# Performance work log

Hardware: AMD Instinct MI355X
Metric: run time of the kernel (lower is better)

The kernel has to match this reference:

```python
import jax, jax.numpy as jnp
import numpy as np

B, S, D, H, FF = 2, 4096, 512, 8, 2048
HD = D // H
EPS = 1e-5


def setup_inputs() -> dict:
    key = jax.random.key(0)
    ks = jax.random.split(key, 14)
    init = lambda k, shape: jax.random.normal(k, shape, dtype=jnp.float32) * 0.02
    return {
        "x": jax.random.normal(ks[0], (B, S, D), dtype=jnp.float32),
        "Wq": init(ks[1], (D, D)), "bq": jnp.zeros((D,), jnp.float32),
        "Wk": init(ks[2], (D, D)), "bk": jnp.zeros((D,), jnp.float32),
        "Wv": init(ks[3], (D, D)), "bv": jnp.zeros((D,), jnp.float32),
        "Wo": init(ks[4], (D, D)), "bo": jnp.zeros((D,), jnp.float32),
        "W1": init(ks[5], (D, FF)), "b1": jnp.zeros((FF,), jnp.float32),
        "W2": init(ks[6], (FF, D)), "b2": jnp.zeros((D,), jnp.float32),
        "g1": jnp.ones((D,), jnp.float32), "beta1": jnp.zeros((D,), jnp.float32),
        "g2": jnp.ones((D,), jnp.float32), "beta2": jnp.zeros((D,), jnp.float32),
    }


def layer_norm(x, g, b):
    mu = jnp.mean(x, axis=-1, keepdims=True)
    var = jnp.mean(jnp.square(x - mu), axis=-1, keepdims=True)
    return (x - mu) * jax.lax.rsqrt(var + EPS) * g + b


def reference(x, Wq, bq, Wk, bk, Wv, bv, Wo, bo, W1, b1, W2, b2, g1, beta1, g2, beta2):
    # --- pre-LN self-attention block ---
    residual = x
    h = layer_norm(x, g1, beta1)
    # project and split heads: [B, H, S, HD]
    q = (h @ Wq + bq).reshape(B, S, H, HD).transpose(0, 2, 1, 3)
    k = (h @ Wk + bk).reshape(B, S, H, HD).transpose(0, 2, 1, 3)
    v = (h @ Wv + bv).reshape(B, S, H, HD).transpose(0, 2, 1, 3)
    scale = HD ** -0.5
    scores = jnp.einsum('bhqd,bhkd->bhqk', q, k) * scale  # [B,H,S,S] materialized
    attn = jax.nn.softmax(scores, axis=-1)
    ctx = jnp.einsum('bhqk,bhkd->bhqd', attn, v)
    ctx = ctx.transpose(0, 2, 1, 3).reshape(B, S, D)
    attn_out = ctx @ Wo + bo
    x = residual + attn_out  # dropout p=0.0 -> identity
    # --- pre-LN FFN block ---
    residual = x
    h = layer_norm(x, g2, beta2)
    h = jax.nn.gelu(h @ W1 + b1, approximate=False)  # nn.GELU default = exact erf
    h = h @ W2 + b2
    x = residual + h
    return (x, attn)
```

## Files before the change

### kernel.cpp

```cpp
#include <hip/hip_runtime.h>
#include <hip/hip_bf16.h>

#define B_ 2
#define S_ 4096
#define D_ 512
#define H_ 8
#define HD_ 64
#define FF_ 2048
#define NT_ (B_*S_)
#define EPS_ 1e-5f

typedef __attribute__((ext_vector_type(8))) short bf16x8;
typedef __attribute__((ext_vector_type(4))) float f32x4;
typedef __attribute__((ext_vector_type(4))) unsigned int u32x4;

__device__ __forceinline__ short f2bf(float f){
  __hip_bfloat16 h = __float2bfloat16(f);
  return __builtin_bit_cast(short, h);
}
__device__ __forceinline__ float bf2f(short s){
  return __bfloat162float(__builtin_bit_cast(__hip_bfloat16, s));
}
__device__ __forceinline__ unsigned pack2(float lo, float hi){
  return ((unsigned)(unsigned short)f2bf(hi) << 16) | (unsigned short)f2bf(lo);
}
__device__ __forceinline__ void load8(const float* p, float* f){
  f32x4 a = *(const f32x4*)p; f32x4 b = *(const f32x4*)(p+4);
  #pragma unroll
  for (int j=0;j<4;j++){ f[j]=a[j]; f[4+j]=b[j]; }
}
__device__ __forceinline__ void load8(const short* p, float* f){
  bf16x8 v = *(const bf16x8*)p;
  #pragma unroll
  for (int j=0;j<8;j++) f[j]=bf2f(v[j]);
}
__device__ __forceinline__ float ldval(const float* p, size_t i){ return p[i]; }
__device__ __forceinline__ float ldval(const short* p, size_t i){ return bf2f(p[i]); }
__device__ __forceinline__ void stval(float* p, size_t i, float v){ p[i]=v; }
__device__ __forceinline__ void stval(short* p, size_t i, float v){ p[i]=f2bf(v); }

#define GLL(src, dst) __builtin_amdgcn_global_load_lds( \
    (const __attribute__((address_space(1))) void*)(src), \
    (__attribute__((address_space(3))) void*)(dst), 16, 0, 0)

__global__ __launch_bounds__(256) void transpose_bf(const float* __restrict__ W,
                                                    short* __restrict__ WT, int K, int N){
  __shared__ float tile[32][33];
  int n0 = blockIdx.x*32, k0 = blockIdx.y*32;
  int tx = threadIdx.x, ty = threadIdx.y;
  #pragma unroll
  for (int i=0;i<32;i+=8)
    tile[ty+i][tx] = W[(size_t)(k0+ty+i)*N + n0+tx];
  __syncthreads();
  #pragma unroll
  for (int i=0;i<32;i+=8)
    WT[(size_t)(n0+ty+i)*K + k0+tx] = f2bf(tile[tx][ty+i]);
}

__global__ __launch_bounds__(256) void transpose_v(const short* __restrict__ V,
                                                   short* __restrict__ VT){
  __shared__ short tile[32][33];
  int d0 = blockIdx.x*32, s0 = blockIdx.y*32, bh = blockIdx.z;
  int b = bh >> 3, h = bh & (H_-1);
  const short* Vp = V + (size_t)b*S_*D_ + (size_t)h*HD_;
  short* VTp = VT + (size_t)bh*HD_*S_;
  int tx = threadIdx.x, ty = threadIdx.y;
  #pragma unroll
  for (int i=0;i<32;i+=8)
    tile[ty+i][tx] = Vp[(size_t)(s0+ty+i)*D_ + d0+tx];
  __syncthreads();
  #pragma unroll
  for (int i=0;i<32;i+=8)
    VTp[(size_t)(d0+ty+i)*S_ + s0+tx] = tile[tx][ty+i];
}

template<typename TIn>
__global__ __launch_bounds__(256) void ln_kernel(const TIn* __restrict__ X,
                                                 const float* __restrict__ G,
                                                 const float* __restrict__ Bt,
                                                 short* __restrict__ O){
  int wid = threadIdx.x>>6, lane = threadIdx.x&63;
  int tok = blockIdx.x*4 + wid;
  const TIn* xp = X + (size_t)tok*D_;
  float f[8]; load8(xp + lane*8, f);
  float s=0.f, s2=0.f;
  #pragma unroll
  for (int j=0;j<8;j++){ s+=f[j]; s2+=f[j]*f[j]; }
  #pragma unroll
  for (int m=1;m<64;m<<=1){ s += __shfl_xor(s,m); s2 += __shfl_xor(s2,m); }
  float mu = s*(1.f/D_);
  float var = s2*(1.f/D_) - mu*mu;
  float rr = rsqrtf(var + EPS_);
  f32x4 g0 = *(const f32x4*)(G + lane*8), g1v = *(const f32x4*)(G + lane*8 + 4);
  f32x4 b0 = *(const f32x4*)(Bt + lane*8), b1v = *(const f32x4*)(Bt + lane*8 + 4);
  bf16x8 o;
  #pragma unroll
  for (int j=0;j<4;j++){
    o[j]   = f2bf((f[j]-mu)*rr*g0[j]  + b0[j]);
    o[4+j] = f2bf((f[4+j]-mu)*rr*g1v[j] + b1v[j]);
  }
  *(bf16x8*)(O + (size_t)tok*D_ + lane*8) = o;
}

template<int EPI, typename TR, typename TO>
__global__ __launch_bounds__(256) void gemm_bt(const short* __restrict__ A,
                                               const short* __restrict__ BT,
                                               const float* __restrict__ bias,
                                               const TR* __restrict__ res,
                                               TO* __restrict__ out,
                                               int M, int N, int K){
  __shared__ short As[128][40];
  __shared__ short Bs[128][40];
  int m0 = blockIdx.y*128, n0 = blockIdx.x*128;
  int tid = threadIdx.x, lane = tid&63, wid = tid>>6;
  int wr = wid>>1, wc = wid&1;
  int r = lane&15, kk = (lane>>4)*8;
  int arow = tid>>2, acol = (tid&3)*8;
  f32x4 zero = {0.f,0.f,0.f,0.f};
  f32x4 acc[4][4];
  #pragma unroll
  for (int i=0;i<4;i++)
    #pragma unroll
    for (int j=0;j<4;j++) acc[i][j] = zero;

  for (int k0=0;k0<K;k0+=32){
    __syncthreads();
    *(bf16x8*)&As[arow][acol]    = *(const bf16x8*)&A [(size_t)(m0+arow)*K    + k0+acol];
    *(bf16x8*)&As[arow+64][acol] = *(const bf16x8*)&A [(size_t)(m0+arow+64)*K + k0+acol];
    *(bf16x8*)&Bs[arow][acol]    = *(const bf16x8*)&BT[(size_t)(n0+arow)*K    + k0+acol];
    *(bf16x8*)&Bs[arow+64][acol] = *(const bf16x8*)&BT[(size_t)(n0+arow+64)*K + k0+acol];
    __syncthreads();
    bf16x8 a[4], b[4];
    #pragma unroll
    for (int i=0;i<4;i++) a[i] = *(const bf16x8*)&As[wr*64+i*16+r][kk];
    #pragma unroll
    for (int i=0;i<4;i++) b[i] = *(const bf16x8*)&Bs[wc*64+i*16+r][kk];
    #pragma unroll
    for (int mi=0;mi<4;mi++)
      #pragma unroll
      for (int ni=0;ni<4;ni++)
        acc[mi][ni] = __builtin_amdgcn_mfma_f32_16x16x32_bf16(a[mi], b[ni], acc[mi][ni], 0,0,0);
  }
  #pragma unroll
  for (int mi=0;mi<4;mi++){
    #pragma unroll
    for (int ni=0;ni<4;ni++){
      int col = n0 + wc*64 + ni*16 + r;
      float bs = bias[col];
      #pragma unroll
      for (int j=0;j<4;j++){
        int row = m0 + wr*64 + mi*16 + (lane>>4)*4 + j;
        float v = acc[mi][ni][j] + bs;
        if (EPI==1) v += ldval(res, (size_t)row*N + col);
        if (EPI==2) v = 0.5f*v*(1.f + erff(v*0.70710678118f));
        stval(out, (size_t)row*N + col, v);
      }
    }
  }
}

__global__ __launch_bounds__(256, 2) void attn_kernel(const short* __restrict__ Q,
                                                      const short* __restrict__ Kt,
                                                      const short* __restrict__ VT,
                                                      float* __restrict__ attn_o,
                                                      short* __restrict__ ctx){
  __shared__ __align__(16) char smem[65536];
  __shared__ float dcomb[4][4][16];
  int wid = threadIdx.x>>6, lane = threadIdx.x&63;
  int bh = blockIdx.y, b = bh>>3, h = bh&7;
  int q0 = blockIdx.x*64;
  int koff = wid*1024;
  int r = lane&15, qh = lane>>4;
  bool hi4 = (lane>>4)&1, hi5 = (lane>>5)&1;
  const short* Qp = Q  + (size_t)b*S_*D_ + (size_t)h*HD_;
  const short* Kp = Kt + (size_t)b*S_*D_ + (size_t)h*HD_;
  const short* Vp = VT + (size_t)bh*HD_*S_;
  float* Ap = attn_o + (size_t)bh*S_*S_;

  char* stg = smem + wid*16384;
  short* KB0 = (short*)stg;         short* KB1 = (short*)(stg+4096);
  short* VB0 = (short*)(stg+8192);  short* VB1 = (short*)(stg+12288);

  auto stageK = [&](int sc, short* buf){
    #pragma unroll
    for (int i=0;i<4;i++){
      int row = i*8 + (lane>>3);
      int col = ((lane&7)*8) ^ ((row&7)*8);
      GLL(&Kp[(size_t)(sc+row)*D_ + col], buf + i*512);
    }
  };
  auto stageV = [&](int sc, short* buf){
    #pragma unroll
    for (int i=0;i<4;i++){
      int d = i*16 + (lane>>2);
      int col = ((lane&3)*8) ^ ((d&3)*8);
      GLL(&Vp[(size_t)d*S_ + sc + col], buf + i*512);
    }
  };
  const int kc0 = (qh*16) ^ ((r&7)<<4);
  const int kc1 = (64 + qh*16) ^ ((r&7)<<4);
  const int vc  = (qh*16) ^ ((r&3)<<4);

  bf16x8 aq[4][2];
  #pragma unroll
  for (int qt=0;qt<4;qt++){
    aq[qt][0] = *(const bf16x8*)&Qp[(size_t)(q0+qt*16+r)*D_ + qh*8];
    aq[qt][1] = *(const bf16x8*)&Qp[(size_t)(q0+qt*16+r)*D_ + 32 + qh*8];
  }
  const f32x4 zero = {0.f,0.f,0.f,0.f};

  float part[4] = {0.f,0.f,0.f,0.f};

#define S1BODY(n, NW, DOSTG) { \
  asm volatile("s_waitcnt vmcnt(" #NW ")" ::: "memory"); \
  short* kb_ = ((n)&1)? KB1 : KB0; \
  bf16x8 kf0 = *(const bf16x8*)((char*)kb_ + r*128 + kc0); \
  bf16x8 kf1 = *(const bf16x8*)((char*)kb_ + r*128 + kc1); \
  bf16x8 kf2 = *(const bf16x8*)((char*)kb_ + (16+r)*128 + kc0); \
  bf16x8 kf3 = *(const bf16x8*)((char*)kb_ + (16+r)*128 + kc1); \
  asm volatile("s_waitcnt lgkmcnt(0)" ::: "memory"); \
  if (DOSTG) stageK(koff + ((n)+2)*32, kb_); \
  _Pragma("unroll") \
  for (int qt=0;qt<4;qt++){ \
    f32x4 s0 = __builtin_amdgcn_mfma_f32_16x16x32_bf16(kf0, aq[qt][0], zero, 0,0,0); \
    s0 = __builtin_amdgcn_mfma_f32_16x16x32_bf16(kf1, aq[qt][1], s0, 0,0,0); \
    f32x4 s1 = __builtin_amdgcn_mfma_f32_16x16x32_bf16(kf2, aq[qt][0], zero, 0,0,0); \
    s1 = __builtin_amdgcn_mfma_f32_16x16x32_bf16(kf3, aq[qt][1], s1, 0,0,0); \
    _Pragma("unroll") \
    for (int j=0;j<4;j++) part[qt] += __expf(s0[j]*0.125f) + __expf(s1[j]*0.125f); \
  } \
}

  stageK(koff, KB0); stageK(koff+32, KB1);
  S1BODY(0,4,1)
  for (int k2=0;k2<14;k2++){ S1BODY(2*k2+1,4,1) S1BODY(2*k2+2,4,1) }
  S1BODY(29,4,1) S1BODY(30,4,0) S1BODY(31,0,0)

  #pragma unroll
  for (int qt=0;qt<4;qt++){
    part[qt] += __shfl_xor(part[qt],16);
    part[qt] += __shfl_xor(part[qt],32);
  }
  if (lane < 16){
    #pragma unroll
    for (int qt=0;qt<4;qt++) dcomb[wid][qt][r] = part[qt];
  }
  __syncthreads();
  float invl[4];
  #pragma unroll
  for (int qt=0;qt<4;qt++)
    invl[qt] = 1.f/(dcomb[0][qt][r]+dcomb[1][qt][r]+dcomb[2][qt][r]+dcomb[3][qt][r]);

  f32x4 cacc[4][4];
  #pragma unroll
  for (int qt=0;qt<4;qt++)
    #pragma unroll
    for (int n2=0;n2<4;n2++) cacc[qt][n2] = zero;

#define S2BODY(n, NW, DOSTG) { \
  asm volatile("s_waitcnt vmcnt(" #NW ")" ::: "memory"); \
  short* kb_ = ((n)&1)? KB1 : KB0; \
  short* vb_ = ((n)&1)? VB1 : VB0; \
  int sc_ = koff + (n)*32; \
  bf16x8 kf0 = *(const bf16x8*)((char*)kb_ + r*128 + kc0); \
  bf16x8 kf1 = *(const bf16x8*)((char*)kb_ + r*128 + kc1); \
  bf16x8 kf2 = *(const bf16x8*)((char*)kb_ + (16+r)*128 + kc0); \
  bf16x8 kf3 = *(const bf16x8*)((char*)kb_ + (16+r)*128 + kc1); \
  bf16x8 vf0 = *(const bf16x8*)((char*)vb_ + (r)*64    + vc); \
  bf16x8 vf1 = *(const bf16x8*)((char*)vb_ + (16+r)*64 + vc); \
  bf16x8 vf2 = *(const bf16x8*)((char*)vb_ + (32+r)*64 + vc); \
  bf16x8 vf3 = *(const bf16x8*)((char*)vb_ + (48+r)*64 + vc); \
  asm volatile("s_waitcnt lgkmcnt(0)" ::: "memory"); \
  if (DOSTG){ stageK(koff+((n)+2)*32, kb_); stageV(koff+((n)+2)*32, vb_); } \
  _Pragma("unroll") \
  for (int qt=0;qt<4;qt++){ \
    f32x4 s0 = __builtin_amdgcn_mfma_f32_16x16x32_bf16(kf0, aq[qt][0], zero, 0,0,0); \
    s0 = __builtin_amdgcn_mfma_f32_16x16x32_bf16(kf1, aq[qt][1], s0, 0,0,0); \
    f32x4 s1 = __builtin_amdgcn_mfma_f32_16x16x32_bf16(kf2, aq[qt][0], zero, 0,0,0); \
    s1 = __builtin_amdgcn_mfma_f32_16x16x32_bf16(kf3, aq[qt][1], s1, 0,0,0); \
    float e0[4], e1[4]; \
    _Pragma("unroll") \
    for (int j=0;j<4;j++){ \
      e0[j] = __expf(s0[j]*0.125f)*invl[qt]; \
      e1[j] = __expf(s1[j]*0.125f)*invl[qt]; \
    } \
    f32x4 o0 = {e0[0],e0[1],e0[2],e0[3]}; \
    f32x4 o1 = {e1[0],e1[1],e1[2],e1[3]}; \
    float* dst = &Ap[(size_t)(q0+qt*16+r)*S_ + sc_ + qh*4]; \
    *(f32x4*)dst = o0; \
    *(f32x4*)(dst+16) = o1; \
    unsigned v0 = pack2(e0[0],e0[1]), v1 = pack2(e0[2],e0[3]); \
    unsigned v2 = pack2(e1[0],e1[1]), v3 = pack2(e1[2],e1[3]); \
    unsigned u0 = __shfl_xor((int)v0,16), u1 = __shfl_xor((int)v1,16); \
    unsigned u2 = __shfl_xor((int)v2,16), u3 = __shfl_xor((int)v3,16); \
    unsigned s0c0 = hi4?u0:v0, s0c1 = hi4?u1:v1, s0c2 = hi4?v0:u0, s0c3 = hi4?v1:u1; \
    unsigned s1c0 = hi4?u2:v2, s1c1 = hi4?u3:v3, s1c2 = hi4?v2:u2, s1c3 = hi4?v3:u3; \
    unsigned w0 = hi5?s0c0:s1c0, w1 = hi5?s0c1:s1c1, w2 = hi5?s0c2:s1c2, w3 = hi5?s0c3:s1c3; \
    unsigned wp0 = __shfl_xor((int)w0,32), wp1 = __shfl_xor((int)w1,32); \
    unsigned wp2 = __shfl_xor((int)w2,32), wp3 = __shfl_xor((int)w3,32); \
    u32x4 pw; \
    pw[0] = (qh==0)?s0c0:(qh==3)?s1c0:wp0; \
    pw[1] = (qh==0)?s0c1:(qh==3)?s1c1:wp1; \
    pw[2] = (qh==0)?s0c2:(qh==3)?s1c2:wp2; \
    pw[3] = (qh==0)?s0c3:(qh==3)?s1c3:wp3; \
    bf16x8 pa = __builtin_bit_cast(bf16x8, pw); \
    cacc[qt][0] = __builtin_amdgcn_mfma_f32_16x16x32_bf16(pa, vf0, cacc[qt][0], 0,0,0); \
    cacc[qt][1] = __builtin_amdgcn_mfma_f32_16x16x32_bf16(pa, vf1, cacc[qt][1], 0,0,0); \
    cacc[qt][2] = __builtin_amdgcn_mfma_f32_16x16x32_bf16(pa, vf2, cacc[qt][2], 0,0,0); \
    cacc[qt][3] = __builtin_amdgcn_mfma_f32_16x16x32_bf16(pa, vf3, cacc[qt][3], 0,0,0); \
  } \
}

  stageK(koff, KB0); stageV(koff, VB0);
  stageK(koff+32, KB1); stageV(koff+32, VB1);
  S2BODY(0,8,1)
  for (int k2=0;k2<14;k2++){ S2BODY(2*k2+1,16,1) S2BODY(2*k2+2,16,1) }
  S2BODY(29,16,1) S2BODY(30,16,0) S2BODY(31,8,0)

  __syncthreads();
  float* cmb = (float*)smem;
  if (wid & 1){
    float* dstp = cmb + (wid>>1)*4096;
    #pragma unroll
    for (int qt=0;qt<4;qt++)
      #pragma unroll
      for (int n2=0;n2<4;n2++)
        #pragma unroll
        for (int j=0;j<4;j++)
          dstp[(qt*16+qh*4+j)*64 + n2*16 + r] = cacc[qt][n2][j];
  }
  __syncthreads();
  if (!(wid & 1)){
    float* srcp = cmb + (wid>>1)*4096;
    #pragma unroll
    for (int qt=0;qt<4;qt++)
      #pragma unroll
      for (int n2=0;n2<4;n2++)
        #pragma unroll
        for (int j=0;j<4;j++)
          cacc[qt][n2][j] += srcp[(qt*16+qh*4+j)*64 + n2*16 + r];
  }
  __syncthreads();
  if (wid == 2){
    #pragma unroll
    for (int qt=0;qt<4;qt++)
      #pragma unroll
      for (int n2=0;n2<4;n2++)
        #pragma unroll
        for (int j=0;j<4;j++)
          cmb[(qt*16+qh*4+j)*64 + n2*16 + r] = cacc[qt][n2][j];
  }
  __syncthreads();
  if (wid == 0){
    #pragma unroll
    for (int qt=0;qt<4;qt++)
      #pragma unroll
      for (int n2=0;n2<4;n2++)
        #pragma unroll
        for (int j=0;j<4;j++){
          float v = cacc[qt][n2][j] + cmb[(qt*16+qh*4+j)*64 + n2*16 + r];
          ctx[(size_t)(b*S_ + q0 + qt*16 + qh*4 + j)*D_ + h*HD_ + n2*16 + r] = f2bf(v);
        }
  }
}

extern "C" void kernel_launch(void* const* d_in, const int* in_sizes, int n_in,
                              void* d_out, int out_size, void* d_ws, size_t ws_size,
                              hipStream_t stream){
  const float* x   = (const float*)d_in[0];
  const float* Wq  = (const float*)d_in[1];
  const float* bq  = (const float*)d_in[2];
  const float* Wk  = (const float*)d_in[3];
  const float* bk  = (const float*)d_in[4];
  const float* Wv  = (const float*)d_in[5];
  const float* bv  = (const float*)d_in[6];
  const float* Wo  = (const float*)d_in[7];
  const float* bo  = (const float*)d_in[8];
  const float* W1  = (const float*)d_in[9];
  const float* b1  = (const float*)d_in[10];
  const float* W2  = (const float*)d_in[11];
  const float* b2  = (const float*)d_in[12];
  const float* g1  = (const float*)d_in[13];
  const float* be1 = (const float*)d_in[14];
  const float* g2  = (const float*)d_in[15];
  const float* be2 = (const float*)d_in[16];

  char* ws = (char*)d_ws;
  const size_t KB = 1024;
  short* wqT = (short*)(ws + 0*KB);
  short* wkT = (short*)(ws + 512*KB);
  short* wvT = (short*)(ws + 1024*KB);
  short* woT = (short*)(ws + 1536*KB);
  short* w1T = (short*)(ws + 2048*KB);
  short* w2T = (short*)(ws + 4096*KB);
  short* hbf = (short*)(ws + 6144*KB);
  short* Qb  = (short*)(ws + 14336*KB);
  short* Kb  = (short*)(ws + 22528*KB);
  short* Vb  = (short*)(ws + 30720*KB);
  short* VTb = (short*)(ws + 38912*KB);
  short* ctx = (short*)(ws + 47104*KB);
  short* f1  = (short*)(ws + 14336*KB);

  float* out0 = (float*)d_out;
  float* attn = out0 + (size_t)NT_*D_;

  dim3 tb(32,8);
  transpose_bf<<<dim3(16,16),tb,0,stream>>>(Wq, wqT, 512, 512);
  transpose_bf<<<dim3(16,16),tb,0,stream>>>(Wk, wkT, 512, 512);
  transpose_bf<<<dim3(16,16),tb,0,stream>>>(Wv, wvT, 512, 512);
  transpose_bf<<<dim3(16,16),tb,0,stream>>>(Wo, woT, 512, 512);
  transpose_bf<<<dim3(64,16),tb,0,stream>>>(W1, w1T, 512, 2048);
  transpose_bf<<<dim3(16,64),tb,0,stream>>>(W2, w2T, 2048, 512);

  ln_kernel<float><<<NT_/4, 256, 0, stream>>>(x, g1, be1, hbf);

  gemm_bt<0,float,short><<<dim3(4,64),256,0,stream>>>(hbf, wqT, bq, nullptr, Qb, NT_, 512, 512);
  gemm_bt<0,float,short><<<dim3(4,64),256,0,stream>>>(hbf, wkT, bk, nullptr, Kb, NT_, 512, 512);
  gemm_bt<0,float,short><<<dim3(4,64),256,0,stream>>>(hbf, wvT, bv, nullptr, Vb, NT_, 512, 512);

  transpose_v<<<dim3(2,128,16),tb,0,stream>>>(Vb, VTb);

  attn_kernel<<<dim3(64,16), 256, 0, stream>>>(Qb, Kb, VTb, attn, ctx);

  gemm_bt<1,float,float><<<dim3(4,64),256,0,stream>>>(ctx, woT, bo, x, out0, NT_, 512, 512);

  ln_kernel<float><<<NT_/4, 256, 0, stream>>>(out0, g2, be2, hbf);

  gemm_bt<2,float,short><<<dim3(16,64),256,0,stream>>>(hbf, w1T, b1, nullptr, f1, NT_, 2048, 512);

  gemm_bt<1,float,float><<<dim3(4,64),256,0,stream>>>(f1, w2T, b2, out0, out0, NT_, 512, 2048);
}
```

Before: 578.5 us.

## Share K/V tiles across two query groups in attention; use async swizzled LDS loads in GEMM

The attention kernel now runs 512 threads per block covering 128 queries. Two groups of four waves share the same K/V staging buffers, with each group loading half of every tile and block-level barriers separating load and use. This halves the global K/V traffic per query, at the cost of extra barriers and changed vmcnt bookkeeping. The GEMM switches to direct global-to-LDS loads with an XOR-swizzled 64-wide K tile, reducing loop iterations and bank conflicts.

```diff
diff --git a/kernel.cpp b/kernel.cpp
--- a/kernel.cpp
+++ b/kernel.cpp
@@ -109,13 +109,14 @@
                                                const TR* __restrict__ res,
                                                TO* __restrict__ out,
                                                int M, int N, int K){
-  __shared__ short As[128][40];
-  __shared__ short Bs[128][40];
+  __shared__ __align__(16) short As[128*64];
+  __shared__ __align__(16) short Bs[128*64];
   int m0 = blockIdx.y*128, n0 = blockIdx.x*128;
   int tid = threadIdx.x, lane = tid&63, wid = tid>>6;
   int wr = wid>>1, wc = wid&1;
-  int r = lane&15, kk = (lane>>4)*8;
-  int arow = tid>>2, acol = (tid&3)*8;
+  int r = lane&15, qh = lane>>4;
+  int srow = wid*32 + (lane>>3);
+  int scole = ((lane&7)*8);
   f32x4 zero = {0.f,0.f,0.f,0.f};
   f32x4 acc[4][4];
   #pragma unroll
@@ -123,23 +124,32 @@
     #pragma unroll
     for (int j=0;j<4;j++) acc[i][j] = zero;
 
-  for (int k0=0;k0<K;k0+=32){
+  for (int k0=0;k0<K;k0+=64){
     __syncthreads();
-    *(bf16x8*)&As[arow][acol]    = *(const bf16x8*)&A [(size_t)(m0+arow)*K    + k0+acol];
-    *(bf16x8*)&As[arow+64][acol] = *(const bf16x8*)&A [(size_t)(m0+arow+64)*K + k0+acol];
-    *(bf16x8*)&Bs[arow][acol]    = *(const bf16x8*)&BT[(size_t)(n0+arow)*K    + k0+acol];
-    *(bf16x8*)&Bs[arow+64][acol] = *(const bf16x8*)&BT[(size_t)(n0+arow+64)*K + k0+acol];
+    #pragma unroll
+    for (int i=0;i<4;i++){
+      int row = srow + i*8;
+      int cole = scole ^ ((row&7)*8);
+      GLL(&A [(size_t)(m0+row)*K + k0 + cole], As + (size_t)(wid*32+i*8)*64);
+      GLL(&BT[(size_t)(n0+row)*K + k0 + cole], Bs + (size_t)(wid*32+i*8)*64);
+    }
     __syncthreads();
-    bf16x8 a[4], b[4];
-    #pragma unroll
-    for (int i=0;i<4;i++) a[i] = *(const bf16x8*)&As[wr*64+i*16+r][kk];
-    #pragma unroll
-    for (int i=0;i<4;i++) b[i] = *(const bf16x8*)&Bs[wc*64+i*16+r][kk];
-    #pragma unroll
-    for (int mi=0;mi<4;mi++)
-      #pragma unroll
-      for (int ni=0;ni<4;ni++)
-        acc[mi][ni] = __builtin_amdgcn_mfma_f32_16x16x32_bf16(a[mi], b[ni], acc[mi][ni], 0,0,0);
+    #pragma unroll
+    for (int half=0; half<2; half++){
+      bf16x8 a[4], b[4];
+      #pragma unroll
+      for (int i=0;i<4;i++){
+        int ar = wr*64+i*16+r;
+        a[i] = *(const bf16x8*)((const char*)As + (size_t)ar*128 + ((qh*16+half*64) ^ ((ar&7)*16)));
+        int br = wc*64+i*16+r;
+        b[i] = *(const bf16x8*)((const char*)Bs + (size_t)br*128 + ((qh*16+half*64) ^ ((br&7)*16)));
+      }
+      #pragma unroll
+      for (int mi=0;mi<4;mi++)
+        #pragma unroll
+        for (int ni=0;ni<4;ni++)
+          acc[mi][ni] = __builtin_amdgcn_mfma_f32_16x16x32_bf16(a[mi], b[ni], acc[mi][ni], 0,0,0);
+    }
   }
   #pragma unroll
   for (int mi=0;mi<4;mi++){
@@ -159,17 +169,19 @@
   }
 }
 
-__global__ __launch_bounds__(256, 2) void attn_kernel(const short* __restrict__ Q,
+__global__ __launch_bounds__(512, 2) void attn_kernel(const short* __restrict__ Q,
                                                       const short* __restrict__ Kt,
                                                       const short* __restrict__ VT,
                                                       float* __restrict__ attn_o,
                                                       short* __restrict__ ctx){
   __shared__ __align__(16) char smem[65536];
-  __shared__ float dcomb[4][4][16];
+  __shared__ float dcomb[8][4][16];
   int wid = threadIdx.x>>6, lane = threadIdx.x&63;
+  int kq = wid&3, rh = wid>>2;
   int bh = blockIdx.y, b = bh>>3, h = bh&7;
-  int q0 = blockIdx.x*64;
-  int koff = wid*1024;
+  int q0 = blockIdx.x*128;
+  int qbase = q0 + rh*64;
+  int koff = kq*1024;
   int r = lane&15, qh = lane>>4;
   bool hi4 = (lane>>4)&1, hi5 = (lane>>5)&1;
   const short* Qp = Q  + (size_t)b*S_*D_ + (size_t)h*HD_;
@@ -177,13 +189,14 @@
   const short* Vp = VT + (size_t)bh*HD_*S_;
   float* Ap = attn_o + (size_t)bh*S_*S_;
 
-  char* stg = smem + wid*16384;
+  char* stg = smem + kq*16384;
   short* KB0 = (short*)stg;         short* KB1 = (short*)(stg+4096);
   short* VB0 = (short*)(stg+8192);  short* VB1 = (short*)(stg+12288);
 
   auto stageK = [&](int sc, short* buf){
     #pragma unroll
-    for (int i=0;i<4;i++){
+    for (int ii=0;ii<2;ii++){
+      int i = rh*2 + ii;
       int row = i*8 + (lane>>3);
       int col = ((lane&7)*8) ^ ((row&7)*8);
       GLL(&Kp[(size_t)(sc+row)*D_ + col], buf + i*512);
@@ -191,7 +204,8 @@
   };
   auto stageV = [&](int sc, short* buf){
     #pragma unroll
-    for (int i=0;i<4;i++){
+    for (int ii=0;ii<2;ii++){
+      int i = rh*2 + ii;
       int d = i*16 + (lane>>2);
       int col = ((lane&3)*8) ^ ((d&3)*8);
       GLL(&Vp[(size_t)d*S_ + sc + col], buf + i*512);
@@ -204,8 +218,8 @@
   bf16x8 aq[4][2];
   #pragma unroll
   for (int qt=0;qt<4;qt++){
-    aq[qt][0] = *(const bf16x8*)&Qp[(size_t)(q0+qt*16+r)*D_ + qh*8];
-    aq[qt][1] = *(const bf16x8*)&Qp[(size_t)(q0+qt*16+r)*D_ + 32 + qh*8];
+    aq[qt][0] = *(const bf16x8*)&Qp[(size_t)(qbase+qt*16+r)*D_ + qh*8];
+    aq[qt][1] = *(const bf16x8*)&Qp[(size_t)(qbase+qt*16+r)*D_ + 32 + qh*8];
   }
   const f32x4 zero = {0.f,0.f,0.f,0.f};
 
@@ -213,12 +227,14 @@
 
 #define S1BODY(n, NW, DOSTG) { \
   asm volatile("s_waitcnt vmcnt(" #NW ")" ::: "memory"); \
+  __builtin_amdgcn_s_barrier(); \
   short* kb_ = ((n)&1)? KB1 : KB0; \
   bf16x8 kf0 = *(const bf16x8*)((char*)kb_ + r*128 + kc0); \
   bf16x8 kf1 = *(const bf16x8*)((char*)kb_ + r*128 + kc1); \
   bf16x8 kf2 = *(const bf16x8*)((char*)kb_ + (16+r)*128 + kc0); \
   bf16x8 kf3 = *(const bf16x8*)((char*)kb_ + (16+r)*128 + kc1); \
   asm volatile("s_waitcnt lgkmcnt(0)" ::: "memory"); \
+  __builtin_amdgcn_s_barrier(); \
   if (DOSTG) stageK(koff + ((n)+2)*32, kb_); \
   _Pragma("unroll") \
   for (int qt=0;qt<4;qt++){ \
@@ -232,9 +248,10 @@
 }
 
   stageK(koff, KB0); stageK(koff+32, KB1);
-  S1BODY(0,4,1)
-  for (int k2=0;k2<14;k2++){ S1BODY(2*k2+1,4,1) S1BODY(2*k2+2,4,1) }
-  S1BODY(29,4,1) S1BODY(30,4,0) S1BODY(31,0,0)
+  S1BODY(0,2,1)
+  for (int k2=0;k2<14;k2++){ S1BODY(2*k2+1,2,1) S1BODY(2*k2+2,2,1) }
+  S1BODY(29,2,1) S1BODY(30,2,0) S1BODY(31,0,0)
+#undef S1BODY
 
   #pragma unroll
   for (int qt=0;qt<4;qt++){
@@ -248,8 +265,11 @@
   __syncthreads();
   float invl[4];
   #pragma unroll
-  for (int qt=0;qt<4;qt++)
-    invl[qt] = 1.f/(dcomb[0][qt][r]+dcomb[1][qt][r]+dcomb[2][qt][r]+dcomb[3][qt][r]);
+  for (int qt=0;qt<4;qt++){
+    float s = dcomb[rh*4+0][qt][r] + dcomb[rh*4+1][qt][r]
+            + dcomb[rh*4+2][qt][r] + dcomb[rh*4+3][qt][r];
+    invl[qt] = 1.f/s;
+  }
 
   f32x4 cacc[4][4];
   #pragma unroll
@@ -259,6 +279,7 @@
 
 #define S2BODY(n, NW, DOSTG) { \
   asm volatile("s_waitcnt vmcnt(" #NW ")" ::: "memory"); \
+  __builtin_amdgcn_s_barrier(); \
   short* kb_ = ((n)&1)? KB1 : KB0; \
   short* vb_ = ((n)&1)? VB1 : VB0; \
   int sc_ = koff + (n)*32; \
@@ -271,6 +292,7 @@
   bf16x8 vf2 = *(const bf16x8*)((char*)vb_ + (32+r)*64 + vc); \
   bf16x8 vf3 = *(const bf16x8*)((char*)vb_ + (48+r)*64 + vc); \
   asm volatile("s_waitcnt lgkmcnt(0)" ::: "memory"); \
+  __builtin_amdgcn_s_barrier(); \
   if (DOSTG){ stageK(koff+((n)+2)*32, kb_); stageV(koff+((n)+2)*32, vb_); } \
   _Pragma("unroll") \
   for (int qt=0;qt<4;qt++){ \
@@ -286,7 +308,7 @@
     } \
     f32x4 o0 = {e0[0],e0[1],e0[2],e0[3]}; \
     f32x4 o1 = {e1[0],e1[1],e1[2],e1[3]}; \
-    float* dst = &Ap[(size_t)(q0+qt*16+r)*S_ + sc_ + qh*4]; \
+    float* dst = &Ap[(size_t)(qbase+qt*16+r)*S_ + sc_ + qh*4]; \
     *(f32x4*)dst = o0; \
     *(f32x4*)(dst+16) = o1; \
     unsigned v0 = pack2(e0[0],e0[1]), v1 = pack2(e0[2],e0[3]); \
@@ -313,14 +335,18 @@
 
   stageK(koff, KB0); stageV(koff, VB0);
   stageK(koff+32, KB1); stageV(koff+32, VB1);
-  S2BODY(0,8,1)
-  for (int k2=0;k2<14;k2++){ S2BODY(2*k2+1,16,1) S2BODY(2*k2+2,16,1) }
-  S2BODY(29,16,1) S2BODY(30,16,0) S2BODY(31,8,0)
+  S2BODY(0,4,1)
+  S2BODY(1,12,1)
+  S2BODY(2,20,1)
+  for (int k2=0;k2<13;k2++){ S2BODY(2*k2+3,20,1) S2BODY(2*k2+4,20,1) }
+  S2BODY(29,20,1) S2BODY(30,20,0) S2BODY(31,16,0)
+#undef S2BODY
 
   __syncthreads();
   float* cmb = (float*)smem;
-  if (wid & 1){
-    float* dstp = cmb + (wid>>1)*4096;
+  float* base = cmb + (size_t)rh*8192;
+  if (kq & 1){
+    float* dstp = base + (size_t)(kq>>1)*4096;
     #pragma unroll
     for (int qt=0;qt<4;qt++)
       #pragma unroll
@@ -330,8 +356,8 @@
           dstp[(qt*16+qh*4+j)*64 + n2*16 + r] = cacc[qt][n2][j];
   }
   __syncthreads();
-  if (!(wid & 1)){
-    float* srcp = cmb + (wid>>1)*4096;
+  if (!(kq & 1)){
+    float* srcp = base + (size_t)(kq>>1)*4096;
     #pragma unroll
     for (int qt=0;qt<4;qt++)
       #pragma unroll
@@ -341,25 +367,25 @@
           cacc[qt][n2][j] += srcp[(qt*16+qh*4+j)*64 + n2*16 + r];
   }
   __syncthreads();
-  if (wid == 2){
+  if (kq == 2){
     #pragma unroll
     for (int qt=0;qt<4;qt++)
       #pragma unroll
       for (int n2=0;n2<4;n2++)
         #pragma unroll
         for (int j=0;j<4;j++)
-          cmb[(qt*16+qh*4+j)*64 + n2*16 + r] = cacc[qt][n2][j];
-  }
-  __syncthreads();
-  if (wid == 0){
+          base[(qt*16+qh*4+j)*64 + n2*16 + r] = cacc[qt][n2][j];
+  }
+  __syncthreads();
+  if (kq == 0){
     #pragma unroll
     for (int qt=0;qt<4;qt++)
       #pragma unroll
       for (int n2=0;n2<4;n2++)
         #pragma unroll
         for (int j=0;j<4;j++){
-          float v = cacc[qt][n2][j] + cmb[(qt*16+qh*4+j)*64 + n2*16 + r];
-          ctx[(size_t)(b*S_ + q0 + qt*16 + qh*4 + j)*D_ + h*HD_ + n2*16 + r] = f2bf(v);
+          float v = cacc[qt][n2][j] + base[(qt*16+qh*4+j)*64 + n2*16 + r];
+          ctx[(size_t)(b*S_ + qbase + qt*16 + qh*4 + j)*D_ + h*HD_ + n2*16 + r] = f2bf(v);
         }
   }
 }
@@ -420,7 +446,7 @@
 
   transpose_v<<<dim3(2,128,16),tb,0,stream>>>(Vb, VTb);
 
-  attn_kernel<<<dim3(64,16), 256, 0, stream>>>(Qb, Kb, VTb, attn, ctx);
+  attn_kernel<<<dim3(32,16), 512, 0, stream>>>(Qb, Kb, VTb, attn, ctx);
 
   gemm_bt<1,float,float><<<dim3(4,64),256,0,stream>>>(ctx, woT, bo, x, out0, NT_, 512, 512);
 
```

Measured after the change: 602.1 us. 4.1% more time.
